# Performance work log

Hardware: AMD Instinct MI355X
Metric: run time of the kernel (lower is better)

## Reference

```python
import math
import jax, jax.numpy as jnp
import numpy as np

B, S, H = 4, 2048, 1024

def setup_inputs() -> dict:
    key = jax.random.key(0)
    k1, k2, k3, k4 = jax.random.split(key, 4)
    X = jax.random.normal(k1, (B, S, H), dtype=jnp.float32)
    attention_mask = jax.random.randint(k2, (B, S), 0, 2).astype(jnp.bool_)
    W = jax.random.normal(k3, (H, 3 * H), dtype=jnp.float32) * (1.0 / math.sqrt(H))
    b = jax.random.normal(k4, (3 * H,), dtype=jnp.float32) * 0.02
    return {"X": X, "attention_mask": attention_mask, "W": W, "b": b}

def reference(X, attention_mask, W, b):
    hidden_dim = X.shape[-1]
    # fused QKV projection: (B,S,3H)
    QKV = X @ W + b
    Q, K, V = jnp.split(QKV, 3, axis=-1)
    # scores: (B, S, S)
    scores = jnp.einsum('bqd,bkd->bqk', Q, K) / math.sqrt(hidden_dim)
    # 2D key-padding mask (B,S) -> broadcast over query dim; True = masked
    mask = attention_mask[:, None, :]  # (B,1,S) broadcasts to (B,S,S)
    scores = jnp.where(mask, -jnp.inf, scores)
    attn = jax.nn.softmax(scores, axis=-1)
    # dropout_rate = 0.0 (eval): identity
    return jnp.einsum('bqk,bkd->bqd', attn, V)
```

## Files before the change

### kernel.cpp

```cpp
#include <hip/hip_runtime.h>
#include <hip/hip_bf16.h>
#include <stdint.h>


typedef __attribute__((ext_vector_type(8))) short bf16x8;
typedef __attribute__((ext_vector_type(4))) float f32x4;

__device__ __forceinline__ void async_cp16(const void* g, void* l) {
  __builtin_amdgcn_global_load_lds(
      (const __attribute__((address_space(1))) void*)g,
      (__attribute__((address_space(3))) void*)l, 16, 0, 0);
}

__device__ __forceinline__ uint32_t laddr(const void* p) {
  return (uint32_t)(uintptr_t)(const __attribute__((address_space(3))) void*)p;
}

#define FENCE() asm volatile("" ::: "memory")
#define BAR()                           \
  do {                                  \
    FENCE();                            \
    __builtin_amdgcn_s_barrier();       \
    FENCE();                            \
  } while (0)
#define VMW(N) asm volatile("s_waitcnt vmcnt(" #N ")" ::: "memory")
#define LGKM0()                                            \
  do {                                                     \
    asm volatile("s_waitcnt lgkmcnt(0)" ::: "memory");     \
    __builtin_amdgcn_sched_barrier(0);                     \
  } while (0)
#define DSR(dst, a, OFF) \
  asm volatile("ds_read_b128 %0, %1 offset:" #OFF : "=v"(dst) : "v"(a))

__global__ __launch_bounds__(256) void prep(
    const float* __restrict__ X, __hip_bfloat16* __restrict__ Xb,
    const float* __restrict__ W, __hip_bfloat16* __restrict__ Wt,
    const int* __restrict__ mask, int* __restrict__ idx,
    int* __restrict__ cnt, int* __restrict__ cnt_pad,
    float* __restrict__ rowsum) {
  const int b = blockIdx.x;
  const int tid = threadIdx.x;
  if (b < 8192) {
    int i = (b * 256 + tid) * 4;
    float4 f = *(const float4*)(X + i);
    __hip_bfloat16 o[4];
    o[0] = __float2bfloat16(f.x);
    o[1] = __float2bfloat16(f.y);
    o[2] = __float2bfloat16(f.z);
    o[3] = __float2bfloat16(f.w);
    *(ushort4*)(Xb + i) = *(const ushort4*)o;
    return;
  }
  if (b < 11264) {
    __shared__ float tile[32][33];
    const int t = b - 8192;
    const int bx = (t % 96) * 32;
    const int by = (t / 96) * 32;
    const int tx = tid & 31, ty = tid >> 5;
#pragma unroll
    for (int j = 0; j < 4; ++j)
      tile[ty + j * 8][tx] = W[(int64_t)(by + ty + j * 8) * 3072 + bx + tx];
    __syncthreads();
#pragma unroll
    for (int j = 0; j < 4; ++j)
      Wt[(int64_t)(bx + ty + j * 8) * 1024 + by + tx] =
          __float2bfloat16(tile[tx][ty + j * 8]);
    return;
  }
  {
    const int z = b - 11264;
    const int* mz = mask + z * 2048;
    int* iz = idx + z * 2048;
    const int lane = tid & 63, wave = tid >> 6;
    float* rs = rowsum + z * 2048;
#pragma unroll
    for (int j = 0; j < 8; ++j) rs[tid + j * 256] = 0.f;

    int keep[8];
    int local = 0;
#pragma unroll
    for (int j = 0; j < 8; ++j) {
      keep[j] = (mz[tid * 8 + j] == 0);
      local += keep[j];
    }
    int pre = local;
#pragma unroll
    for (int off = 1; off <= 32; off <<= 1) {
      int n = __shfl_up(pre, off, 64);
      if (lane >= off) pre += n;
    }
    __shared__ int wsum[4];
    if (lane == 63) wsum[wave] = pre;
    __syncthreads();
    int base = 0;
    for (int w = 0; w < wave; ++w) base += wsum[w];
    int excl = base + pre - local;
#pragma unroll
    for (int j = 0; j < 8; ++j)
      if (keep[j]) iz[excl++] = tid * 8 + j;
    if (tid == 255) {
      int tot = base + pre;
      cnt[z] = tot;
      cnt_pad[z] = (tot + 127) & ~127;
    }
  }
}

__global__ __launch_bounds__(256) void gemm_qkv(
    const __hip_bfloat16* __restrict__ Xb, const __hip_bfloat16* __restrict__ Wt,
    const float* __restrict__ bias, const int* __restrict__ idx,
    const int* __restrict__ cnt, const int* __restrict__ cnt_pad,
    __hip_bfloat16* __restrict__ Q, __hip_bfloat16* __restrict__ Kc,
    __hip_bfloat16* __restrict__ Vt) {
  const int z = blockIdx.z;
  const int f = blockIdx.x;
  const int xcd = f & 7, loc = f >> 3;
  const int m0 = ((loc & 7) * 2 + (xcd >> 2)) * 128;
  const int n_idx = (loc >> 3) * 4 + (xcd & 3);
  const bool isQ = (n_idx < 8);
  if (!isQ && m0 >= cnt_pad[z]) return;
  const int n0 = (isQ ? n_idx : n_idx - 8) * 128;
  const __hip_bfloat16* A = Xb + (int64_t)z * 2048 * 1024;
  const __hip_bfloat16* Bt = Wt + (isQ ? 0 : (int64_t)1024 * 1024);
  const float* bv = bias + (isQ ? 0 : 1024);

  const int tid = threadIdx.x;
  const int wave = tid >> 6, lane = tid & 63;
  const int quad = lane >> 4, tr = lane & 15, t7 = tr & 7;
  const int wm = wave & 1, wn = wave >> 1;

  __shared__ __hip_bfloat16 ls[32768];

  const __hip_bfloat16* gsrc[8];
  int loff[8];
  {
    const int srow = lane >> 3;
    const int kcs = (((lane & 7) ^ srow) * 8);
    const int cz = isQ ? 0 : cnt[z];
    const int* idxz = idx + z * 2048;
#pragma unroll
    for (int cc = 0; cc < 8; ++cc) {
      int c = wave * 8 + cc;
      int isA = (c < 16);
      int cr = isA ? c : (c - 16);
      int row = cr * 8 + srow;
      if (isA) {
        int ar = m0 + row;
        if (!isQ) ar = (ar < cz) ? idxz[ar] : 0;
        gsrc[cc] = A + (int64_t)ar * 1024 + kcs;
      } else {
        gsrc[cc] = Bt + (int64_t)(n0 + row) * 1024 + kcs;
      }
      loff[cc] = (isA ? 0 : 8192) + cr * 512;
    }
  }

  uint32_t aAd[2][2], bBd[2][2];
  {
    uint32_t base = laddr(ls);
#pragma unroll
    for (int b = 0; b < 2; ++b)
#pragma unroll
      for (int w = 0; w < 2; ++w) {
        uint32_t col = (uint32_t)(((((w << 2) | quad)) ^ t7) * 16);
        aAd[b][w] = base + b * 32768 + (wm * 64 + tr) * 128 + col;
        bBd[b][w] = base + b * 32768 + 16384 + (wn * 64 + tr) * 128 + col;
      }
  }

  f32x4 acc[4][4];
#pragma unroll
  for (int mi = 0; mi < 4; ++mi)
#pragma unroll
    for (int ni = 0; ni < 4; ++ni) acc[mi][ni] = (f32x4){0.f, 0.f, 0.f, 0.f};

  bf16x8 af[4], bf[4];

#define STAGE(BUF, k0)                                            \
  do {                                                            \
    _Pragma("unroll") for (int cc = 0; cc < 8; ++cc)              \
        async_cp16(gsrc[cc] + (k0), ls + (BUF)*16384 + loff[cc]); \
  } while (0)
#define COMP(BUF)                                                             \
  do {                                                                        \
    _Pragma("unroll") for (int w = 0; w < 2; ++w) {                           \
      DSR(af[0], aAd[BUF][w], 0);                                             \
      DSR(af[1], aAd[BUF][w], 2048);                                          \
      DSR(af[2], aAd[BUF][w], 4096);                                          \
      DSR(af[3], aAd[BUF][w], 6144);                                          \
      DSR(bf[0], bBd[BUF][w], 0);                                             \
      DSR(bf[1], bBd[BUF][w], 2048);                                          \
      DSR(bf[2], bBd[BUF][w], 4096);                                          \
      DSR(bf[3], bBd[BUF][w], 6144);                                          \
      LGKM0();                                                                \
      _Pragma("unroll") for (int mi = 0; mi < 4; ++mi)                        \
          _Pragma("unroll") for (int ni = 0; ni < 4; ++ni) acc[mi][ni] =      \
              __builtin_amdgcn_mfma_f32_16x16x32_bf16(af[mi], bf[ni],         \
                                                      acc[mi][ni], 0, 0, 0);  \
    }                                                                         \
  } while (0)

  STAGE(0, 0);
  for (int it = 0; it < 8; ++it) {
    STAGE(1, (2 * it + 1) * 64);
    VMW(8); BAR();
    COMP(0);
    BAR();
    if (it < 7) {
      STAGE(0, (2 * it + 2) * 64);
      VMW(8);
    } else {
      VMW(0);
    }
    BAR();
    COMP(1);
    BAR();
  }
#undef STAGE
#undef COMP

  const int rowbase = m0 + wm * 64;
  const int colbase = n0 + wn * 64;
  if (isQ) {
    __hip_bfloat16* C = Q + (int64_t)z * 2048 * 1024;
#pragma unroll
    for (int ni = 0; ni < 4; ++ni) {
      int col = colbase + ni * 16 + tr;
      float bb = bv[col];
#pragma unroll
      for (int mi = 0; mi < 4; ++mi) {
        int row = rowbase + mi * 16 + quad * 4;
#pragma unroll
        for (int r = 0; r < 4; ++r)
          C[(int64_t)(row + r) * 1024 + col] =
              __float2bfloat16(acc[mi][ni][r] + bb);
      }
    }
  } else if (n0 < 1024) {
    __hip_bfloat16* C = Kc + (int64_t)z * 2048 * 1024;
#pragma unroll
    for (int ni = 0; ni < 4; ++ni) {
      int col = colbase + ni * 16 + tr;
      float bb = bv[col];
#pragma unroll
      for (int mi = 0; mi < 4; ++mi) {
        int row = rowbase + mi * 16 + quad * 4;
#pragma unroll
        for (int r = 0; r < 4; ++r)
          C[(int64_t)(row + r) * 1024 + col] =
              __float2bfloat16(acc[mi][ni][r] + bb);
      }
    }
  } else {
    __syncthreads();
#pragma unroll
    for (int ni = 0; ni < 4; ++ni) {
      int cl = wn * 64 + ni * 16 + tr;
      float bb = bv[colbase + ni * 16 + tr];
#pragma unroll
      for (int mi = 0; mi < 4; ++mi) {
        int rl = wm * 64 + mi * 16 + quad * 4;
        __hip_bfloat16 h[4];
#pragma unroll
        for (int r = 0; r < 4; ++r) h[r] = __float2bfloat16(acc[mi][ni][r] + bb);
        *(ushort4*)(ls + cl * 136 + rl) = *(const ushort4*)h;
      }
    }
    __syncthreads();
    __hip_bfloat16* Vz = Vt + (int64_t)z * 1024 * 2048;
    const int d0 = n0 - 1024;
    const int seg = tid & 15;
#pragma unroll
    for (int p = 0; p < 8; ++p) {
      int d = p * 16 + (tid >> 4);
      bf16x8 v = *(const bf16x8*)(ls + d * 136 + seg * 8);
      *(bf16x8*)(Vz + (int64_t)(d0 + d) * 2048 + m0 + seg * 8) = v;
    }
  }
}

__global__ __launch_bounds__(256) void gemm_scores(
    const __hip_bfloat16* __restrict__ Qb, const __hip_bfloat16* __restrict__ Kc,
    __hip_bfloat16* __restrict__ Sc, float* __restrict__ rowsum,
    const int* __restrict__ cnt, const int* __restrict__ cnt_pad,
    float scale2) {
  const int z = blockIdx.z;
  const int f = blockIdx.x;
  const int xcd = f & 7, loc = f >> 3;
  const int m0 = ((loc & 7) * 2 + (xcd >> 2)) * 128;
  const int n0 = ((loc >> 3) * 4 + (xcd & 3)) * 128;
  if (n0 >= cnt_pad[z]) return;
  const __hip_bfloat16* A = Qb + (int64_t)z * 2048 * 1024;
  const __hip_bfloat16* Bt = Kc + (int64_t)z * 2048 * 1024;

  const int tid = threadIdx.x;
  const int wave = tid >> 6, lane = tid & 63;
  const int quad = lane >> 4, tr = lane & 15, t7 = tr & 7;
  const int wm = wave & 1, wn = wave >> 1;

  __shared__ __hip_bfloat16 ls[32768];

  const __hip_bfloat16* gsrc[8];
  int loff[8];
  {
    const int srow = lane >> 3;
    const int kcs = (((lane & 7) ^ srow) * 8);
#pragma unroll
    for (int cc = 0; cc < 8; ++cc) {
      int c = wave * 8 + cc;
      int isA = (c < 16);
      int cr = isA ? c : (c - 16);
      int row = cr * 8 + srow;
      gsrc[cc] = isA ? (A + (int64_t)(m0 + row) * 1024 + kcs)
                     : (Bt + (int64_t)(n0 + row) * 1024 + kcs);
      loff[cc] = (isA ? 0 : 8192) + cr * 512;
    }
  }

  uint32_t aAd[2][2], bBd[2][2];
  {
    uint32_t base = laddr(ls);
#pragma unroll
    for (int b = 0; b < 2; ++b)
#pragma unroll
      for (int w = 0; w < 2; ++w) {
        uint32_t col = (uint32_t)(((((w << 2) | quad)) ^ t7) * 16);
        aAd[b][w] = base + b * 32768 + (wm * 64 + tr) * 128 + col;
        bBd[b][w] = base + b * 32768 + 16384 + (wn * 64 + tr) * 128 + col;
      }
  }

  f32x4 acc[4][4];
#pragma unroll
  for (int mi = 0; mi < 4; ++mi)
#pragma unroll
    for (int ni = 0; ni < 4; ++ni) acc[mi][ni] = (f32x4){0.f, 0.f, 0.f, 0.f};

  bf16x8 af[4], bf[4];

#define STAGE(BUF, k0)                                            \
  do {                                                            \
    _Pragma("unroll") for (int cc = 0; cc < 8; ++cc)              \
        async_cp16(gsrc[cc] + (k0), ls + (BUF)*16384 + loff[cc]); \
  } while (0)
#define COMP(BUF)                                                             \
  do {                                                                        \
    _Pragma("unroll") for (int w = 0; w < 2; ++w) {                           \
      DSR(af[0], aAd[BUF][w], 0);                                             \
      DSR(af[1], aAd[BUF][w], 2048);                                          \
      DSR(af[2], aAd[BUF][w], 4096);                                          \
      DSR(af[3], aAd[BUF][w], 6144);                                          \
      DSR(bf[0], bBd[BUF][w], 0);                                             \
      DSR(bf[1], bBd[BUF][w], 2048);                                          \
      DSR(bf[2], bBd[BUF][w], 4096);                                          \
      DSR(bf[3], bBd[BUF][w], 6144);                                          \
      LGKM0();                                                                \
      _Pragma("unroll") for (int mi = 0; mi < 4; ++mi)                        \
          _Pragma("unroll") for (int ni = 0; ni < 4; ++ni) acc[mi][ni] =      \
              __builtin_amdgcn_mfma_f32_16x16x32_bf16(af[mi], bf[ni],         \
                                                      acc[mi][ni], 0, 0, 0);  \
    }                                                                         \
  } while (0)

  STAGE(0, 0);
  for (int it = 0; it < 8; ++it) {
    STAGE(1, (2 * it + 1) * 64);
    VMW(8); BAR();
    COMP(0);
    BAR();
    if (it < 7) {
      STAGE(0, (2 * it + 2) * 64);
      VMW(8);
    } else {
      VMW(0);
    }
    BAR();
    COMP(1);
    BAR();
  }
#undef STAGE
#undef COMP

  const int rowbase = m0 + wm * 64;
  const int colbase = n0 + wn * 64;
  const int cn = cnt[z];
  __hip_bfloat16* C = Sc + (int64_t)z * 2048 * 2048;

  float psum[4][4];
#pragma unroll
  for (int mi = 0; mi < 4; ++mi)
#pragma unroll
    for (int r = 0; r < 4; ++r) psum[mi][r] = 0.f;

#pragma unroll
  for (int ni = 0; ni < 4; ++ni) {
    int col = colbase + ni * 16 + tr;
    bool valid = (col < cn);
#pragma unroll
    for (int mi = 0; mi < 4; ++mi) {
      int row = rowbase + mi * 16 + quad * 4;
#pragma unroll
      for (int r = 0; r < 4; ++r) {
        float e = valid ? exp2f(acc[mi][ni][r] * scale2) : 0.f;
        C[(int64_t)(row + r) * 2048 + col] = __float2bfloat16(e);
        psum[mi][r] += e;
      }
    }
  }
#pragma unroll
  for (int off = 1; off <= 8; off <<= 1)
#pragma unroll
    for (int mi = 0; mi < 4; ++mi)
#pragma unroll
      for (int r = 0; r < 4; ++r)
        psum[mi][r] += __shfl_xor(psum[mi][r], off, 64);
  if (tr == 0) {
    float* rs = rowsum + z * 2048 + rowbase;
#pragma unroll
    for (int mi = 0; mi < 4; ++mi)
#pragma unroll
      for (int r = 0; r < 4; ++r)
        atomicAdd(&rs[mi * 16 + quad * 4 + r], psum[mi][r]);
  }
}

__global__ __launch_bounds__(256) void gemm_pv(
    const __hip_bfloat16* __restrict__ Sc, const __hip_bfloat16* __restrict__ Vt,
    float* __restrict__ out, const float* __restrict__ rowsum,
    const int* __restrict__ cnt_pad) {
  const int z = blockIdx.z;
  const int f = blockIdx.x;
  const int xcd = f & 7, loc = f >> 3;
  const int m0 = ((loc & 7) * 2 + (xcd >> 2)) * 128;
  const int n0 = ((loc >> 3) * 4 + (xcd & 3)) * 128;
  const int Ks = cnt_pad[z];
  const __hip_bfloat16* A = Sc + (int64_t)z * 2048 * 2048;
  const __hip_bfloat16* Bt = Vt + (int64_t)z * 1024 * 2048;

  const int tid = threadIdx.x;
  const int wave = tid >> 6, lane = tid & 63;
  const int quad = lane >> 4, tr = lane & 15, t7 = tr & 7;
  const int wm = wave & 1, wn = wave >> 1;

  __shared__ __hip_bfloat16 ls[32768];

  const __hip_bfloat16* gsrc[8];
  int loff[8];
  {
    const int srow = lane >> 3;
    const int kcs = (((lane & 7) ^ srow) * 8);
#pragma unroll
    for (int cc = 0; cc < 8; ++cc) {
      int c = wave * 8 + cc;
      int isA = (c < 16);
      int cr = isA ? c : (c - 16);
      int row = cr * 8 + srow;
      gsrc[cc] = isA ? (A + (int64_t)(m0 + row) * 2048 + kcs)
                     : (Bt + (int64_t)(n0 + row) * 2048 + kcs);
      loff[cc] = (isA ? 0 : 8192) + cr * 512;
    }
  }

  uint32_t aAd[2][2], bBd[2][2];
  {
    uint32_t base = laddr(ls);
#pragma unroll
    for (int b = 0; b < 2; ++b)
#pragma unroll
      for (int w = 0; w < 2; ++w) {
        uint32_t col = (uint32_t)(((((w << 2) | quad)) ^ t7) * 16);
        aAd[b][w] = base + b * 32768 + (wm * 64 + tr) * 128 + col;
        bBd[b][w] = base + b * 32768 + 16384 + (wn * 64 + tr) * 128 + col;
      }
  }

  f32x4 acc[4][4];
#pragma unroll
  for (int mi = 0; mi < 4; ++mi)
#pragma unroll
    for (int ni = 0; ni < 4; ++ni) acc[mi][ni] = (f32x4){0.f, 0.f, 0.f, 0.f};

  bf16x8 af[4], bf[4];

#define STAGE(BUF, k0)                                            \
  do {                                                            \
    _Pragma("unroll") for (int cc = 0; cc < 8; ++cc)              \
        async_cp16(gsrc[cc] + (k0), ls + (BUF)*16384 + loff[cc]); \
  } while (0)
#define COMP(BUF)                                                             \
  do {                                                                        \
    _Pragma("unroll") for (int w = 0; w < 2; ++w) {                           \
      DSR(af[0], aAd[BUF][w], 0);                                             \
      DSR(af[1], aAd[BUF][w], 2048);                                          \
      DSR(af[2], aAd[BUF][w], 4096);                                          \
      DSR(af[3], aAd[BUF][w], 6144);                                          \
      DSR(bf[0], bBd[BUF][w], 0);                                             \
      DSR(bf[1], bBd[BUF][w], 2048);                                          \
      DSR(bf[2], bBd[BUF][w], 4096);                                          \
      DSR(bf[3], bBd[BUF][w], 6144);                                          \
      LGKM0();                                                                \
      _Pragma("unroll") for (int mi = 0; mi < 4; ++mi)                        \
          _Pragma("unroll") for (int ni = 0; ni < 4; ++ni) acc[mi][ni] =      \
              __builtin_amdgcn_mfma_f32_16x16x32_bf16(af[mi], bf[ni],         \
                                                      acc[mi][ni], 0, 0, 0);  \
    }                                                                         \
  } while (0)

  const int NP = Ks >> 7;
  STAGE(0, 0);
  for (int it = 0; it < NP; ++it) {
    STAGE(1, (2 * it + 1) * 64);
    VMW(8); BAR();
    COMP(0);
    BAR();
    if (it + 1 < NP) {
      STAGE(0, (2 * it + 2) * 64);
      VMW(8);
    } else {
      VMW(0);
    }
    BAR();
    COMP(1);
    BAR();
  }
#undef STAGE
#undef COMP

  const int rowbase = m0 + wm * 64;
  const int colbase = n0 + wn * 64;
  const float* rs = rowsum + z * 2048 + rowbase;
  float invv[4][4];
#pragma unroll
  for (int mi = 0; mi < 4; ++mi)
#pragma unroll
    for (int r = 0; r < 4; ++r) invv[mi][r] = 1.0f / rs[mi * 16 + quad * 4 + r];

  float* C = out + (int64_t)z * 2048 * 1024;
#pragma unroll
  for (int ni = 0; ni < 4; ++ni) {
    int col = colbase + ni * 16 + tr;
#pragma unroll
    for (int mi = 0; mi < 4; ++mi) {
      int row = rowbase + mi * 16 + quad * 4;
#pragma unroll
      for (int r = 0; r < 4; ++r)
        C[(int64_t)(row + r) * 1024 + col] = acc[mi][ni][r] * invv[mi][r];
    }
  }
}

extern "C" void kernel_launch(void* const* d_in, const int* in_sizes, int n_in,
                              void* d_out, int out_size, void* d_ws,
                              size_t ws_size, hipStream_t stream) {
  const float* X = (const float*)d_in[0];
  const int* mask = (const int*)d_in[1];
  const float* W = (const float*)d_in[2];
  const float* bias = (const float*)d_in[3];
  float* out = (float*)d_out;

  char* ws = (char*)d_ws;
  auto alloc = [&](size_t bytes) {
    char* p = ws;
    ws += (bytes + 255) & ~(size_t)255;
    return p;
  };
  __hip_bfloat16* Xb = (__hip_bfloat16*)alloc(8192ULL * 1024 * 2);
  __hip_bfloat16* Wt = (__hip_bfloat16*)alloc(3072ULL * 1024 * 2);
  __hip_bfloat16* Q = (__hip_bfloat16*)alloc(8192ULL * 1024 * 2);
  __hip_bfloat16* Kc = (__hip_bfloat16*)alloc(4ULL * 2048 * 1024 * 2);
  __hip_bfloat16* Vt = (__hip_bfloat16*)alloc(4ULL * 1024 * 2048 * 2);
  __hip_bfloat16* Sc = (__hip_bfloat16*)alloc(4ULL * 2048 * 2048 * 2);
  float* rowsum = (float*)alloc(8192ULL * 4);
  int* idx = (int*)alloc(4ULL * 2048 * 4);
  int* cnt = (int*)alloc(64);
  int* cnt_pad = (int*)alloc(64);

  prep<<<11268, 256, 0, stream>>>(X, Xb, W, Wt, mask, idx, cnt, cnt_pad,
                                  rowsum);
  gemm_qkv<<<dim3(384, 1, 4), 256, 0, stream>>>(Xb, Wt, bias, idx, cnt,
                                                cnt_pad, Q, Kc, Vt);
  gemm_scores<<<dim3(256, 1, 4), 256, 0, stream>>>(
      Q, Kc, Sc, rowsum, cnt, cnt_pad, 0.03125f * 1.4426950408889634f);
  gemm_pv<<<dim3(128, 1, 4), 256, 0, stream>>>(Sc, Vt, out, rowsum, cnt_pad);
}
```

Measured before the change: 191.7 us.

## Halve N tile to 64 and single-buffer LDS in scores and PV GEMMs

Shrinks the output tile of the scores and PV GEMMs from 128x128 to 128x64, doubling the grid size of both launches. It also replaces the double-buffered async LDS pipeline with a single 24KB buffer that waits for each K-step to load before computing. Both kernels now declare launch bounds of 4 blocks per unit. The aim is more resident blocks and better load balance, letting occupancy hide memory latency. The cost is less data reuse per tile, more global traffic for the A operand, and no intra-block overlap of loads with MFMA work.

```diff
diff --git a/kernel.cpp b/kernel.cpp
--- a/kernel.cpp
+++ b/kernel.cpp
@@ -279,7 +279,7 @@
   }
 }
 
-__global__ __launch_bounds__(256) void gemm_scores(
+__global__ __launch_bounds__(256, 4) void gemm_scores(
     const __hip_bfloat16* __restrict__ Qb, const __hip_bfloat16* __restrict__ Kc,
     __hip_bfloat16* __restrict__ Sc, float* __restrict__ rowsum,
     const int* __restrict__ cnt, const int* __restrict__ cnt_pad,
@@ -288,7 +288,7 @@
   const int f = blockIdx.x;
   const int xcd = f & 7, loc = f >> 3;
   const int m0 = ((loc & 7) * 2 + (xcd >> 2)) * 128;
-  const int n0 = ((loc >> 3) * 4 + (xcd & 3)) * 128;
+  const int n0 = ((loc >> 3) * 4 + (xcd & 3)) * 64;
   if (n0 >= cnt_pad[z]) return;
   const __hip_bfloat16* A = Qb + (int64_t)z * 2048 * 1024;
   const __hip_bfloat16* Bt = Kc + (int64_t)z * 2048 * 1024;
@@ -298,16 +298,16 @@
   const int quad = lane >> 4, tr = lane & 15, t7 = tr & 7;
   const int wm = wave & 1, wn = wave >> 1;
 
-  __shared__ __hip_bfloat16 ls[32768];
-
-  const __hip_bfloat16* gsrc[8];
-  int loff[8];
+  __shared__ __hip_bfloat16 ls[12288];
+
+  const __hip_bfloat16* gsrc[6];
+  int loff[6];
   {
     const int srow = lane >> 3;
     const int kcs = (((lane & 7) ^ srow) * 8);
 #pragma unroll
-    for (int cc = 0; cc < 8; ++cc) {
-      int c = wave * 8 + cc;
+    for (int cc = 0; cc < 6; ++cc) {
+      int c = wave * 6 + cc;
       int isA = (c < 16);
       int cr = isA ? c : (c - 16);
       int row = cr * 8 + srow;
@@ -317,72 +317,59 @@
     }
   }
 
-  uint32_t aAd[2][2], bBd[2][2];
+  uint32_t aAd[2], bBd[2];
   {
     uint32_t base = laddr(ls);
 #pragma unroll
-    for (int b = 0; b < 2; ++b)
-#pragma unroll
-      for (int w = 0; w < 2; ++w) {
-        uint32_t col = (uint32_t)(((((w << 2) | quad)) ^ t7) * 16);
-        aAd[b][w] = base + b * 32768 + (wm * 64 + tr) * 128 + col;
-        bBd[b][w] = base + b * 32768 + 16384 + (wn * 64 + tr) * 128 + col;
-      }
-  }
-
-  f32x4 acc[4][4];
+    for (int w = 0; w < 2; ++w) {
+      uint32_t col = (uint32_t)(((((w << 2) | quad)) ^ t7) * 16);
+      aAd[w] = base + (wm * 64 + tr) * 128 + col;
+      bBd[w] = base + 16384 + (wn * 32 + tr) * 128 + col;
+    }
+  }
+
+  f32x4 acc[4][2];
 #pragma unroll
   for (int mi = 0; mi < 4; ++mi)
 #pragma unroll
-    for (int ni = 0; ni < 4; ++ni) acc[mi][ni] = (f32x4){0.f, 0.f, 0.f, 0.f};
-
-  bf16x8 af[4], bf[4];
-
-#define STAGE(BUF, k0)                                            \
-  do {                                                            \
-    _Pragma("unroll") for (int cc = 0; cc < 8; ++cc)              \
-        async_cp16(gsrc[cc] + (k0), ls + (BUF)*16384 + loff[cc]); \
-  } while (0)
-#define COMP(BUF)                                                             \
+    for (int ni = 0; ni < 2; ++ni) acc[mi][ni] = (f32x4){0.f, 0.f, 0.f, 0.f};
+
+  bf16x8 af[4], bf[2];
+
+#define STAGE(k0)                                     \
+  do {                                                \
+    _Pragma("unroll") for (int cc = 0; cc < 6; ++cc)  \
+        async_cp16(gsrc[cc] + (k0), ls + loff[cc]);   \
+  } while (0)
+#define COMP()                                                                \
   do {                                                                        \
     _Pragma("unroll") for (int w = 0; w < 2; ++w) {                           \
-      DSR(af[0], aAd[BUF][w], 0);                                             \
-      DSR(af[1], aAd[BUF][w], 2048);                                          \
-      DSR(af[2], aAd[BUF][w], 4096);                                          \
-      DSR(af[3], aAd[BUF][w], 6144);                                          \
-      DSR(bf[0], bBd[BUF][w], 0);                                             \
-      DSR(bf[1], bBd[BUF][w], 2048);                                          \
-      DSR(bf[2], bBd[BUF][w], 4096);                                          \
-      DSR(bf[3], bBd[BUF][w], 6144);                                          \
+      DSR(af[0], aAd[w], 0);                                                  \
+      DSR(af[1], aAd[w], 2048);                                               \
+      DSR(af[2], aAd[w], 4096);                                               \
+      DSR(af[3], aAd[w], 6144);                                               \
+      DSR(bf[0], bBd[w], 0);                                                  \
+      DSR(bf[1], bBd[w], 2048);                                               \
       LGKM0();                                                                \
       _Pragma("unroll") for (int mi = 0; mi < 4; ++mi)                        \
-          _Pragma("unroll") for (int ni = 0; ni < 4; ++ni) acc[mi][ni] =      \
+          _Pragma("unroll") for (int ni = 0; ni < 2; ++ni) acc[mi][ni] =      \
               __builtin_amdgcn_mfma_f32_16x16x32_bf16(af[mi], bf[ni],         \
                                                       acc[mi][ni], 0, 0, 0);  \
     }                                                                         \
   } while (0)
 
-  STAGE(0, 0);
-  for (int it = 0; it < 8; ++it) {
-    STAGE(1, (2 * it + 1) * 64);
-    VMW(8); BAR();
-    COMP(0);
-    BAR();
-    if (it < 7) {
-      STAGE(0, (2 * it + 2) * 64);
-      VMW(8);
-    } else {
-      VMW(0);
-    }
-    BAR();
-    COMP(1);
-    BAR();
+  for (int t = 0; t < 16; ++t) {
+    BAR();
+    STAGE(t * 64);
+    VMW(0);
+    BAR();
+    COMP();
   }
 #undef STAGE
 #undef COMP
 
   const int rowbase = m0 + wm * 64;
-  const int colbase = n0 + wn * 64;
+  const int colbase = n0 + wn * 32;
   const int cn = cnt[z];
   __hip_bfloat16* C = Sc + (int64_t)z * 2048 * 2048;
 
@@ -393,7 +380,7 @@
     for (int r = 0; r < 4; ++r) psum[mi][r] = 0.f;
 
 #pragma unroll
-  for (int ni = 0; ni < 4; ++ni) {
+  for (int ni = 0; ni < 2; ++ni) {
     int col = colbase + ni * 16 + tr;
     bool valid = (col < cn);
 #pragma unroll
@@ -424,7 +411,7 @@
   }
 }
 
-__global__ __launch_bounds__(256) void gemm_pv(
+__global__ __launch_bounds__(256, 4) void gemm_pv(
     const __hip_bfloat16* __restrict__ Sc, const __hip_bfloat16* __restrict__ Vt,
     float* __restrict__ out, const float* __restrict__ rowsum,
     const int* __restrict__ cnt_pad) {
@@ -432,7 +419,7 @@
   const int f = blockIdx.x;
   const int xcd = f & 7, loc = f >> 3;
   const int m0 = ((loc & 7) * 2 + (xcd >> 2)) * 128;
-  const int n0 = ((loc >> 3) * 4 + (xcd & 3)) * 128;
+  const int n0 = ((loc >> 3) * 4 + (xcd & 3)) * 64;
   const int Ks = cnt_pad[z];
   const __hip_bfloat16* A = Sc + (int64_t)z * 2048 * 2048;
   const __hip_bfloat16* Bt = Vt + (int64_t)z * 1024 * 2048;
@@ -442,16 +429,16 @@
   const int quad = lane >> 4, tr = lane & 15, t7 = tr & 7;
   const int wm = wave & 1, wn = wave >> 1;
 
-  __shared__ __hip_bfloat16 ls[32768];
-
-  const __hip_bfloat16* gsrc[8];
-  int loff[8];
+  __shared__ __hip_bfloat16 ls[12288];
+
+  const __hip_bfloat16* gsrc[6];
+  int loff[6];
   {
     const int srow = lane >> 3;
     const int kcs = (((lane & 7) ^ srow) * 8);
 #pragma unroll
-    for (int cc = 0; cc < 8; ++cc) {
-      int c = wave * 8 + cc;
+    for (int cc = 0; cc < 6; ++cc) {
+      int c = wave * 6 + cc;
       int isA = (c < 16);
       int cr = isA ? c : (c - 16);
       int row = cr * 8 + srow;
@@ -461,73 +448,60 @@
     }
   }
 
-  uint32_t aAd[2][2], bBd[2][2];
+  uint32_t aAd[2], bBd[2];
   {
     uint32_t base = laddr(ls);
 #pragma unroll
-    for (int b = 0; b < 2; ++b)
-#pragma unroll
-      for (int w = 0; w < 2; ++w) {
-        uint32_t col = (uint32_t)(((((w << 2) | quad)) ^ t7) * 16);
-        aAd[b][w] = base + b * 32768 + (wm * 64 + tr) * 128 + col;
-        bBd[b][w] = base + b * 32768 + 16384 + (wn * 64 + tr) * 128 + col;
-      }
-  }
-
-  f32x4 acc[4][4];
+    for (int w = 0; w < 2; ++w) {
+      uint32_t col = (uint32_t)(((((w << 2) | quad)) ^ t7) * 16);
+      aAd[w] = base + (wm * 64 + tr) * 128 + col;
+      bBd[w] = base + 16384 + (wn * 32 + tr) * 128 + col;
+    }
+  }
+
+  f32x4 acc[4][2];
 #pragma unroll
   for (int mi = 0; mi < 4; ++mi)
 #pragma unroll
-    for (int ni = 0; ni < 4; ++ni) acc[mi][ni] = (f32x4){0.f, 0.f, 0.f, 0.f};
-
-  bf16x8 af[4], bf[4];
-
-#define STAGE(BUF, k0)                                            \
-  do {                                                            \
-    _Pragma("unroll") for (int cc = 0; cc < 8; ++cc)              \
-        async_cp16(gsrc[cc] + (k0), ls + (BUF)*16384 + loff[cc]); \
-  } while (0)
-#define COMP(BUF)                                                             \
+    for (int ni = 0; ni < 2; ++ni) acc[mi][ni] = (f32x4){0.f, 0.f, 0.f, 0.f};
+
+  bf16x8 af[4], bf[2];
+
+#define STAGE(k0)                                     \
+  do {                                                \
+    _Pragma("unroll") for (int cc = 0; cc < 6; ++cc)  \
+        async_cp16(gsrc[cc] + (k0), ls + loff[cc]);   \
+  } while (0)
+#define COMP()                                                                \
   do {                                                                        \
     _Pragma("unroll") for (int w = 0; w < 2; ++w) {                           \
-      DSR(af[0], aAd[BUF][w], 0);                                             \
-      DSR(af[1], aAd[BUF][w], 2048);                                          \
-      DSR(af[2], aAd[BUF][w], 4096);                                          \
-      DSR(af[3], aAd[BUF][w], 6144);                                          \
-      DSR(bf[0], bBd[BUF][w], 0);                                             \
-      DSR(bf[1], bBd[BUF][w], 2048);                                          \
-      DSR(bf[2], bBd[BUF][w], 4096);                                          \
-      DSR(bf[3], bBd[BUF][w], 6144);                                          \
+      DSR(af[0], aAd[w], 0);                                                  \
+      DSR(af[1], aAd[w], 2048);                                               \
+      DSR(af[2], aAd[w], 4096);                                               \
+      DSR(af[3], aAd[w], 6144);                                               \
+      DSR(bf[0], bBd[w], 0);                                                  \
+      DSR(bf[1], bBd[w], 2048);                                               \
       LGKM0();                                                                \
       _Pragma("unroll") for (int mi = 0; mi < 4; ++mi)                        \
-          _Pragma("unroll") for (int ni = 0; ni < 4; ++ni) acc[mi][ni] =      \
+          _Pragma("unroll") for (int ni = 0; ni < 2; ++ni) acc[mi][ni] =      \
               __builtin_amdgcn_mfma_f32_16x16x32_bf16(af[mi], bf[ni],         \
                                                       acc[mi][ni], 0, 0, 0);  \
     }                                                                         \
   } while (0)
 
-  const int NP = Ks >> 7;
-  STAGE(0, 0);
-  for (int it = 0; it < NP; ++it) {
-    STAGE(1, (2 * it + 1) * 64);
-    VMW(8); BAR();
-    COMP(0);
-    BAR();
-    if (it + 1 < NP) {
-      STAGE(0, (2 * it + 2) * 64);
-      VMW(8);
-    } else {
-      VMW(0);
-    }
-    BAR();
-    COMP(1);
-    BAR();
+  const int NT = Ks >> 6;
+  for (int t = 0; t < NT; ++t) {
+    BAR();
+    STAGE(t * 64);
+    VMW(0);
+    BAR();
+    COMP();
   }
 #undef STAGE
 #undef COMP
 
   const int rowbase = m0 + wm * 64;
-  const int colbase = n0 + wn * 64;
+  const int colbase = n0 + wn * 32;
   const float* rs = rowsum + z * 2048 + rowbase;
   float invv[4][4];
 #pragma unroll
@@ -537,7 +511,7 @@
 
   float* C = out + (int64_t)z * 2048 * 1024;
 #pragma unroll
-  for (int ni = 0; ni < 4; ++ni) {
+  for (int ni = 0; ni < 2; ++ni) {
     int col = colbase + ni * 16 + tr;
 #pragma unroll
     for (int mi = 0; mi < 4; ++mi) {
@@ -579,7 +553,7 @@
                                   rowsum);
   gemm_qkv<<<dim3(384, 1, 4), 256, 0, stream>>>(Xb, Wt, bias, idx, cnt,
                                                 cnt_pad, Q, Kc, Vt);
-  gemm_scores<<<dim3(256, 1, 4), 256, 0, stream>>>(
+  gemm_scores<<<dim3(512, 1, 4), 256, 0, stream>>>(
       Q, Kc, Sc, rowsum, cnt, cnt_pad, 0.03125f * 1.4426950408889634f);
-  gemm_pv<<<dim3(128, 1, 4), 256, 0, stream>>>(Sc, Vt, out, rowsum, cnt_pad);
-}
+  gemm_pv<<<dim3(256, 1, 4), 256, 0, stream>>>(Sc, Vt, out, rowsum, cnt_pad);
+}
```

New measurement: 201.5 us. +5.1%, slower.
